# Performance work log

Measured on AMD Instinct MI355X. Metric: run time of the kernel, lower is better.

## Reference

```python
import jax, jax.numpy as jnp
import numpy as np

B, N, K = 8, 2048, 32
EPS = 1e-5


def _lrelu(x):
    return jnp.where(x >= 0, x, 0.2 * x)


def _bn(x, p):
    # inference BatchNorm; x: [B, C, ...], p: [4, C] = (gamma, beta, mean, var)
    g, b, m, v = p[0], p[1], p[2], p[3]
    shape = (1, -1) + (1,) * (x.ndim - 2)
    scale = g * jax.lax.rsqrt(v + EPS)
    return (x - m.reshape(shape)) * scale.reshape(shape) + b.reshape(shape)


def _group(x, k):
    # ops.group with xyz_or_feature='feature', feature_or_diff='diff'
    # x: [B, C, N] -> edge features [B, 2C, N, k] = cat(neighbor - center, center)
    xt = jnp.transpose(x, (0, 2, 1))  # [B, N, C]
    sq = jnp.sum(xt * xt, axis=-1)    # [B, N]
    dist = sq[:, :, None] - 2.0 * jnp.einsum('bnc,bmc->bnm', xt, xt) + sq[:, None, :]
    idx = jax.lax.top_k(-dist, k)[1]  # [B, N, k] nearest neighbors
    nbr = jax.vmap(lambda f, i: f[i])(xt, idx)  # [B, N, k, C]
    center = xt[:, :, None, :]
    edge = jnp.concatenate([nbr - center, jnp.broadcast_to(center, nbr.shape)], axis=-1)
    return jnp.transpose(edge, (0, 3, 1, 2))  # [B, 2C, N, k]


def _edgeconv(x, w1, bn1, w2, bn2, k):
    e = _group(x, k)
    h = _lrelu(_bn(jnp.einsum('oc,bcnk->bonk', w1, e), bn1))
    h = _lrelu(_bn(jnp.einsum('oc,bcnk->bonk', w2, h), bn2))
    return jnp.max(h, axis=-1)  # max over neighbors -> [B, C_out, N]


def _model(x,
           ec1_w1, ec1_bn1, ec1_w2, ec1_bn2,
           ec2_w1, ec2_bn1, ec2_w2, ec2_bn2,
           ec3_w1, ec3_bn1, ec3_w2, ec3_bn2,
           emb_w, q_w, k_w, v_w, att_bn1, ff_w1, ff_w2, att_bn2,
           cb_w, cb_bn):
    # EdgeConvBlock (3 stacked EdgeConvs, outputs concatenated)
    f1 = _edgeconv(x, ec1_w1, ec1_bn1, ec1_w2, ec1_bn2, K)
    f2 = _edgeconv(f1, ec2_w1, ec2_bn1, ec2_w2, ec2_bn2, K)
    f3 = _edgeconv(f2, ec3_w1, ec3_bn1, ec3_w2, ec3_bn2, K)
    xc = jnp.concatenate([f1, f2, f3], axis=1)  # [B, 192, N]
    # Point2PointAttentionBlock: embedding then dense self-attention
    h = jnp.einsum('oc,bcn->bon', emb_w, xc)  # [B, 1024, N]
    q = jnp.einsum('oc,bcn->bon', q_w, h)
    kk = jnp.einsum('oc,bcn->bon', k_w, h)
    v = jnp.einsum('oc,bcn->bon', v_w, h)
    scale = jnp.sqrt(jnp.asarray(h.shape[1], h.dtype))
    att = jax.nn.softmax(jnp.einsum('bcn,bcm->bnm', q, kk) / scale, axis=-1)  # [B, N, N]
    x_r = jnp.einsum('bnm,bcm->bcn', att, v)
    h = _bn(h + x_r, att_bn1)
    ff = jnp.einsum('oc,bcn->bon', ff_w2, _lrelu(jnp.einsum('oc,bcn->bon', ff_w1, h)))
    h = _bn(h + ff, att_bn2)
    # ConvBlock head
    return _lrelu(_bn(jnp.einsum('oc,bcn->bon', cb_w, h), cb_bn))  # [B, 1024, N]


def setup_inputs() -> dict:
    key = jax.random.key(0)
    ks = iter(jax.random.split(key, 32))

    def randn(shape, s=0.1):
        return jax.random.normal(next(ks), shape, jnp.float32) * s

    def bnp(c):
        return jax.random.uniform(next(ks), (4, c), jnp.float32, 0.1, 1.0)

    return {
        'x': randn((B, 3, N), 1.0),
        'ec1_w1': randn((64, 6)), 'ec1_bn1': bnp(64),
        'ec1_w2': randn((64, 64)), 'ec1_bn2': bnp(64),
        'ec2_w1': randn((64, 128)), 'ec2_bn1': bnp(64),
        'ec2_w2': randn((64, 64)), 'ec2_bn2': bnp(64),
        'ec3_w1': randn((64, 128)), 'ec3_bn1': bnp(64),
        'ec3_w2': randn((64, 64)), 'ec3_bn2': bnp(64),
        'emb_w': randn((1024, 192), 0.05),
        'q_w': randn((1024, 1024), 0.03),
        'k_w': randn((1024, 1024), 0.03),
        'v_w': randn((1024, 1024), 0.03),
        'att_bn1': bnp(1024),
        'ff_w1': randn((512, 1024), 0.03),
        'ff_w2': randn((1024, 512), 0.03),
        'att_bn2': bnp(1024),
        'cb_w': randn((1024, 1024), 0.03),
        'cb_bn': bnp(1024),
    }


def reference(x,
              ec1_w1, ec1_bn1, ec1_w2, ec1_bn2,
              ec2_w1, ec2_bn1, ec2_w2, ec2_bn2,
              ec3_w1, ec3_bn1, ec3_w2, ec3_bn2,
              emb_w, q_w, k_w, v_w, att_bn1, ff_w1, ff_w2, att_bn2,
              cb_w, cb_bn):
    return _model(x,
                  ec1_w1, ec1_bn1, ec1_w2, ec1_bn2,
                  ec2_w1, ec2_bn1, ec2_w2, ec2_bn2,
                  ec3_w1, ec3_bn1, ec3_w2, ec3_bn2,
                  emb_w, q_w, k_w, v_w, att_bn1, ff_w1, ff_w2, att_bn2,
                  cb_w, cb_bn)
```

## Files before the change

### kernel.cpp

```cpp
#include <hip/hip_runtime.h>
#include <hip/hip_bf16.h>

constexpr int Bn  = 8;
constexpr int Np  = 2048;
constexpr int KNN = 32;

typedef __attribute__((ext_vector_type(8))) short bf16x8;
typedef __attribute__((ext_vector_type(4))) float f32x4;

__device__ static inline void gll16(const void* g, void* l) {
  __builtin_amdgcn_global_load_lds((const __attribute__((address_space(1))) void*)g,
                                   (__attribute__((address_space(3))) void*)l, 16, 0, 0);
}

__device__ static inline unsigned short f2bf(float x) {
  union { __hip_bfloat16 h; unsigned short u; } cv; cv.h = __float2bfloat16(x); return cv.u;
}
__device__ static inline float bf2f(unsigned short u) {
  union { __hip_bfloat16 h; unsigned short u; } cv; cv.u = u; return __bfloat162float(cv.h);
}

__global__ __launch_bounds__(256)
void cvt_bf16_kernel(const float* __restrict__ s, __hip_bfloat16* __restrict__ d, int n) {
  int i = blockIdx.x * 256 + threadIdx.x;
  if (i < n) d[i] = __float2bfloat16(s[i]);
}

template<int CIN, int K1>
__global__ __launch_bounds__(256)
void cvt_w1a(const float* __restrict__ w1, __hip_bfloat16* __restrict__ out) {
  int i = blockIdx.x * 256 + threadIdx.x;
  if (i >= 64 * K1) return;
  int o = i / K1, c = i - o * K1;
  out[i] = __float2bfloat16(c < CIN ? w1[o * 2 * CIN + c] : 0.f);
}

__global__ __launch_bounds__(256)
void xpose_kernel(const float* __restrict__ x, float* __restrict__ xt,
                  __hip_bfloat16* __restrict__ xb) {
  int i = blockIdx.x * 256 + threadIdx.x;
  int b = i >> 11, n = i & 2047;
  const float* p = x + (long)b * 3 * Np + n;
  float vx = p[0], vy = p[Np], vz = p[2 * Np];
  xt[(long)i * 4 + 0] = vx;
  xt[(long)i * 4 + 1] = vy;
  xt[(long)i * 4 + 2] = vz;
  xt[(long)i * 4 + 3] = 0.f;
  __hip_bfloat16* q = xb + (long)i * 8;
  q[0] = __float2bfloat16(vx); q[1] = __float2bfloat16(vy);
  q[2] = __float2bfloat16(vz);
  q[3] = __float2bfloat16(0.f); q[4] = q[3]; q[5] = q[3]; q[6] = q[3]; q[7] = q[3];
}

template<int C, int CP>
__global__ __launch_bounds__(256)
void sq_kernel(const float* __restrict__ f, float* __restrict__ out) {
  int i = blockIdx.x * 256 + threadIdx.x;
  const float* p = f + (long)i * CP;
  float s = 0.f;
#pragma unroll
  for (int c = 0; c < C; ++c) s += p[c] * p[c];
  out[i] = s;
}

template<int CIN, int CP>
__global__ __launch_bounds__(256)
void split_kernel(const float* __restrict__ f, __hip_bfloat16* __restrict__ fhi,
                  __hip_bfloat16* __restrict__ flo) {
  int i = blockIdx.x * 256 + threadIdx.x;
  int n = i >> 6, c = i & 63;
  float v = (c < CIN) ? f[(long)n * CP + c] : 0.f;
  __hip_bfloat16 h = __float2bfloat16(v);
  fhi[i] = h;
  flo[i] = __float2bfloat16(v - __bfloat162float(h));
}

__device__ static inline unsigned umin32(unsigned a, unsigned b) { return a < b ? a : b; }

__device__ static inline int mbcnt64(unsigned long long m) {
  return __builtin_amdgcn_mbcnt_hi((unsigned)(m >> 32),
         __builtin_amdgcn_mbcnt_lo((unsigned)m, 0u));
}

__device__ static inline unsigned long long shfl64x(unsigned long long k, int m) {
  unsigned lo = (unsigned)__shfl_xor((int)(unsigned)k, m);
  unsigned hi = (unsigned)__shfl_xor((int)(unsigned)(k >> 32), m);
  return ((unsigned long long)hi << 32) | (unsigned long long)lo;
}

__device__ static inline unsigned long long lane_sort64_u64(unsigned long long v, int lane) {
#pragma unroll
  for (int k = 2; k <= 64; k <<= 1) {
#pragma unroll
    for (int j = k >> 1; j > 0; j >>= 1) {
      unsigned long long o = shfl64x(v, j);
      bool dir = ((lane & k) == 0);
      bool lower = ((lane & j) == 0);
      bool keep = (v < o) == (dir == lower);
      v = keep ? v : o;
    }
  }
  return v;
}

__device__ static inline unsigned long long lane_merge64(unsigned long long a,
                                                         unsigned long long b, int lane) {
  unsigned long long br = shfl64x(b, 63);
  unsigned long long m = a < br ? a : br;
#pragma unroll
  for (int j = 32; j > 0; j >>= 1) {
    unsigned long long o = shfl64x(m, j);
    bool lower = ((lane & j) == 0);
    bool keep = (m < o) == lower;
    m = keep ? m : o;
  }
  return m;
}

__device__ static inline unsigned kth_u32(unsigned v, int km1) {
  unsigned p = 0;
#pragma unroll
  for (int b = 31; b >= 0; --b) {
    unsigned t = p | (1u << b);
    if ((int)__popcll(__ballot(v < t)) <= km1) p = t;
  }
  return p;
}

template<int MAP, int CAP>
__device__ static inline void row_topk(const unsigned* val, unsigned long long* cbuf,
                                       int lane, int* outp) {
  unsigned tmn[16];
#pragma unroll
  for (int i = 0; i < 16; ++i) tmn[i] = umin32(val[i], val[i + 16]);
#pragma unroll
  for (int w2 = 8; w2 >= 1; w2 >>= 1)
#pragma unroll
    for (int i = 0; i < 8; ++i)
      if (i < w2) tmn[i] = umin32(tmn[i], tmn[i + w2]);

  unsigned T = kth_u32(tmn[0], 31);

  int S = 0;
#pragma unroll
  for (int s = 0; s < 32; ++s) {
    bool p = val[s] <= T;
    unsigned long long mask = __ballot(p);
    int pos = S + mbcnt64(mask);
    unsigned idx = (MAP == 0) ? (unsigned)((s >> 2) * 256 + lane * 4 + (s & 3))
                              : (unsigned)((s >> 2) * 256 + (s & 3) * 64 + lane);
    if (p && pos < CAP) cbuf[pos] = ((unsigned long long)val[s] << 32) | idx;
    S += (int)__popcll(mask);
  }

  if (S <= 64) {
    unsigned long long k = (lane < S) ? cbuf[lane] : ~0ull;
    unsigned vs = (unsigned)(k >> 32), ix = (unsigned)k;
    unsigned vstar = kth_u32(vs, 31);
    int c1 = (int)__popcll(__ballot(vs < vstar));
    int r = 32 - c1;
    unsigned istar = 0;
#pragma unroll
    for (int b = 10; b >= 0; --b) {
      unsigned t = istar | (1u << b);
      if ((int)__popcll(__ballot(vs == vstar && ix < t)) <= r - 1) istar = t;
    }
    bool sel = (vs < vstar) || (vs == vstar && ix <= istar);
    unsigned long long m = __ballot(sel);
    if (sel) outp[mbcnt64(m)] = (int)ix;
  } else if (S <= CAP) {
    int nslot = (S + 63) >> 6;
    unsigned vs[CAP / 64], is_[CAP / 64];
#pragma unroll
    for (int q = 0; q < CAP / 64; ++q) {
      unsigned long long k = (q * 64 + lane < S) ? cbuf[q * 64 + lane] : ~0ull;
      vs[q] = (unsigned)(k >> 32);
      is_[q] = (unsigned)k;
    }
    unsigned vstar = 0;
#pragma unroll
    for (int b = 31; b >= 0; --b) {
      unsigned t = vstar | (1u << b);
      int c = 0;
      for (int q = 0; q < nslot; ++q) c += (int)__popcll(__ballot(vs[q] < t));
      if (c <= 31) vstar = t;
    }
    int c1 = 0;
    for (int q = 0; q < nslot; ++q) c1 += (int)__popcll(__ballot(vs[q] < vstar));
    int r = 32 - c1;
    unsigned istar = 0;
#pragma unroll
    for (int b = 10; b >= 0; --b) {
      unsigned t = istar | (1u << b);
      int c = 0;
      for (int q = 0; q < nslot; ++q)
        c += (int)__popcll(__ballot(vs[q] == vstar && is_[q] < t));
      if (c <= r - 1) istar = t;
    }
    int base = 0;
    for (int q = 0; q < nslot; ++q) {
      bool sel = (vs[q] < vstar) || (vs[q] == vstar && is_[q] <= istar);
      unsigned long long m = __ballot(sel);
      if (sel) outp[base + mbcnt64(m)] = (int)is_[q];
      base += (int)__popcll(m);
    }
  } else {
    unsigned long long cur = ~0ull;
    for (int s = 0; s < 32; ++s) {
      unsigned idx = (MAP == 0) ? (unsigned)((s >> 2) * 256 + lane * 4 + (s & 3))
                                : (unsigned)((s >> 2) * 256 + (s & 3) * 64 + lane);
      unsigned long long kc = ((unsigned long long)val[s] << 32) | idx;
      cur = lane_merge64(cur, lane_sort64_u64(kc, lane), lane);
    }
    if (lane < KNN) outp[lane] = (int)(unsigned)cur;
  }
}

__global__ __launch_bounds__(512)
void knn3_kernel(const float* __restrict__ xt, const float* __restrict__ sqb,
                 int* __restrict__ idxOut) {
  __shared__ float4 F[2048];
  __shared__ float sqS[2048];
  __shared__ unsigned long long cbuf[8 * 256];
  int t = threadIdx.x, lane = t & 63, w = t >> 6;
  long pb = (long)blockIdx.y * Np;
  for (int e = t; e < 2048; e += 512) {
    F[e] = ((const float4*)xt)[pb + e];
    sqS[e] = sqb[pb + e];
  }
  __syncthreads();
  int row = blockIdx.x * 8 + w;
  float4 a = F[row];
  unsigned val[32];
#pragma unroll
  for (int j4 = 0; j4 < 8; ++j4)
#pragma unroll
    for (int u = 0; u < 4; ++u) {
      int col = j4 * 256 + u * 64 + lane;
      float4 fb = F[col];
      float d = sqS[col] - 2.f * (a.x * fb.x + a.y * fb.y + a.z * fb.z);
      unsigned b = __float_as_uint(d);
      val[j4 * 4 + u] = b ^ ((unsigned)((int)b >> 31) | 0x80000000u);
    }
  row_topk<1, 256>(val, cbuf + w * 256, lane, idxOut + (pb + row) * KNN);
}

__global__ __launch_bounds__(512)
void knn16_kernel(const __hip_bfloat16* __restrict__ fhi,
                  const __hip_bfloat16* __restrict__ flo,
                  const float* __restrict__ sqb, int* __restrict__ idxOut) {
  constexpr int LDW = 2052;
  constexpr int CAP = 256;
  __shared__ __align__(16) float Dw[16 * LDW];
  __shared__ float sqS[2048];
  __shared__ unsigned long long cbuf[8 * CAP];
  int t = threadIdx.x, lane = t & 63, w = t >> 6;
  long pb = (long)blockIdx.y * Np;
  int r0 = blockIdx.x * 16;
  const __hip_bfloat16* fh = fhi + pb * 64;
  const __hip_bfloat16* fl = flo + pb * 64;

  ((float4*)sqS)[t] = ((const float4*)(sqb + pb))[t];

  int ar = r0 + (lane & 15);
  int kc = (lane >> 4) * 8;
  int n15 = lane & 15;
  bf16x8 ah[2], al[2];
#pragma unroll
  for (int k2 = 0; k2 < 2; ++k2) {
    ah[k2] = *(const bf16x8*)(fh + (long)ar * 64 + k2 * 32 + kc);
    al[k2] = *(const bf16x8*)(fl + (long)ar * 64 + k2 * 32 + kc);
  }
  __syncthreads();

  int cb0 = w * 256;
  bf16x8 b0h[2], b0l[2], b1h[2], b1l[2];
  {
    int bc = cb0 + n15;
#pragma unroll
    for (int k2 = 0; k2 < 2; ++k2) {
      b0h[k2] = *(const bf16x8*)(fh + (long)bc * 64 + k2 * 32 + kc);
      b0l[k2] = *(const bf16x8*)(fl + (long)bc * 64 + k2 * 32 + kc);
    }
    bc = cb0 + 16 + n15;
#pragma unroll
    for (int k2 = 0; k2 < 2; ++k2) {
      b1h[k2] = *(const bf16x8*)(fh + (long)bc * 64 + k2 * 32 + kc);
      b1l[k2] = *(const bf16x8*)(fl + (long)bc * 64 + k2 * 32 + kc);
    }
  }
  int m0 = (lane >> 4) * 4;
#pragma unroll
  for (int cp = 0; cp < 8; ++cp) {
    {
      int ct = cp * 2;
      bf16x8 nh[2], nl[2];
      if (ct + 2 < 16) {
        int bc = cb0 + (ct + 2) * 16 + n15;
#pragma unroll
        for (int k2 = 0; k2 < 2; ++k2) {
          nh[k2] = *(const bf16x8*)(fh + (long)bc * 64 + k2 * 32 + kc);
          nl[k2] = *(const bf16x8*)(fl + (long)bc * 64 + k2 * 32 + kc);
        }
      }
      f32x4 acc = f32x4{0.f, 0.f, 0.f, 0.f};
#pragma unroll
      for (int k2 = 0; k2 < 2; ++k2) {
        acc = __builtin_amdgcn_mfma_f32_16x16x32_bf16(ah[k2], b0h[k2], acc, 0, 0, 0);
        acc = __builtin_amdgcn_mfma_f32_16x16x32_bf16(ah[k2], b0l[k2], acc, 0, 0, 0);
        acc = __builtin_amdgcn_mfma_f32_16x16x32_bf16(al[k2], b0h[k2], acc, 0, 0, 0);
      }
      int col = cb0 + ct * 16 + n15;
      float sqv = sqS[col];
#pragma unroll
      for (int r = 0; r < 4; ++r)
        Dw[(m0 + r) * LDW + col] = sqv - 2.f * acc[r];
#pragma unroll
      for (int k2 = 0; k2 < 2; ++k2) { b0h[k2] = nh[k2]; b0l[k2] = nl[k2]; }
    }
    {
      int ct = cp * 2 + 1;
      bf16x8 nh[2], nl[2];
      if (ct + 2 < 16) {
        int bc = cb0 + (ct + 2) * 16 + n15;
#pragma unroll
        for (int k2 = 0; k2 < 2; ++k2) {
          nh[k2] = *(const bf16x8*)(fh + (long)bc * 64 + k2 * 32 + kc);
          nl[k2] = *(const bf16x8*)(fl + (long)bc * 64 + k2 * 32 + kc);
        }
      }
      f32x4 acc = f32x4{0.f, 0.f, 0.f, 0.f};
#pragma unroll
      for (int k2 = 0; k2 < 2; ++k2) {
        acc = __builtin_amdgcn_mfma_f32_16x16x32_bf16(ah[k2], b1h[k2], acc, 0, 0, 0);
        acc = __builtin_amdgcn_mfma_f32_16x16x32_bf16(ah[k2], b1l[k2], acc, 0, 0, 0);
        acc = __builtin_amdgcn_mfma_f32_16x16x32_bf16(al[k2], b1h[k2], acc, 0, 0, 0);
      }
      int col = cb0 + ct * 16 + n15;
      float sqv = sqS[col];
#pragma unroll
      for (int r = 0; r < 4; ++r)
        Dw[(m0 + r) * LDW + col] = sqv - 2.f * acc[r];
#pragma unroll
      for (int k2 = 0; k2 < 2; ++k2) { b1h[k2] = nh[k2]; b1l[k2] = nl[k2]; }
    }
  }
  __syncthreads();

  for (int rr = 0; rr < 2; ++rr) {
    int row = w * 2 + rr;
    unsigned val[32];
    const float4* rp = (const float4*)&Dw[row * LDW];
#pragma unroll
    for (int j4 = 0; j4 < 8; ++j4) {
      float4 f4 = rp[j4 * 64 + lane];
      float fv[4] = {f4.x, f4.y, f4.z, f4.w};
#pragma unroll
      for (int u = 0; u < 4; ++u) {
        unsigned b = __float_as_uint(fv[u]);
        val[j4 * 4 + u] = b ^ ((unsigned)((int)b >> 31) | 0x80000000u);
      }
    }
    row_topk<0, CAP>(val, cbuf + w * CAP, lane, idxOut + (pb + r0 + row) * KNN);
  }
}

template<int CIN, int CP>
__global__ __launch_bounds__(256)
void biasker(const float* __restrict__ feat, const float* __restrict__ w1,
             float* __restrict__ bias) {
  __shared__ float wd[64][CIN + 1];
  int tid = threadIdx.x;
  for (int e = tid; e < 64 * CIN; e += 256) {
    int o = e / CIN, c = e - o * CIN;
    wd[o][c] = w1[o * 2 * CIN + CIN + c] - w1[o * 2 * CIN + c];
  }
  __syncthreads();
  int wv = tid >> 6, o = tid & 63;
  float wr_[CIN];
#pragma unroll
  for (int c = 0; c < CIN; ++c) wr_[c] = wd[o][c];
  long base = (long)blockIdx.y * Np + blockIdx.x * 32 + wv * 8;
  for (int p = 0; p < 8; ++p) {
    const float* fr = feat + (base + p) * CP;
    float acc = 0.f;
#pragma unroll
    for (int c = 0; c < CIN; ++c) acc = fmaf(wr_[c], fr[c], acc);
    bias[(base + p) * 64 + o] = acc;
  }
}

template<int K1>
__global__ __launch_bounds__(256)
void edge_mfma(const __hip_bfloat16* __restrict__ featb, int fstride,
               const int* __restrict__ idx, const float* __restrict__ bias,
               const __hip_bfloat16* __restrict__ w1b,
               const __hip_bfloat16* __restrict__ w2b,
               const float* __restrict__ bn1, const float* __restrict__ bn2,
               float* __restrict__ fout, __hip_bfloat16* __restrict__ xcseg) {
  __shared__ __align__(16) char lds[32768 + 64 * K1 * 2 + 8192 + 1024 + 512];
  __hip_bfloat16* A  = (__hip_bfloat16*)lds;
  __hip_bfloat16* H1 = A + 128 * K1;
  float*          H2 = (float*)lds;
  __hip_bfloat16* W1 = (__hip_bfloat16*)(lds + 32768);
  __hip_bfloat16* W2 = W1 + 64 * K1;
  float* biasS = (float*)(lds + 32768 + 64 * K1 * 2 + 8192);
  int*   idxS  = (int*)(biasS + 256);

  int t = threadIdx.x, lane = t & 63, w = t >> 6;
  long pb = (long)blockIdx.y * Np;
  int p0 = blockIdx.x * 4;

  if (t < 128) idxS[t] = idx[(pb + p0 + (t >> 5)) * KNN + (t & 31)];
  biasS[w * 64 + lane] = bias[(pb + p0 + w) * 64 + lane];
  for (int e = t; e < 64 * K1 / 8; e += 256)
    ((ulonglong2*)W1)[e] = ((const ulonglong2*)w1b)[e];
  for (int e = t; e < 512; e += 256)
    ((ulonglong2*)W2)[e] = ((const ulonglong2*)w2b)[e];
  __syncthreads();

  if (K1 == 64) {
#pragma unroll
    for (int i = 0; i < 4; ++i) {
      int e = t + i * 256;
      int r = e >> 3, cc = e & 7;
      const ulonglong2* src = (const ulonglong2*)(featb + (pb + idxS[r]) * fstride) + cc;
      ((ulonglong2*)(A + r * 64))[cc] = *src;
    }
  } else {
    if (t < 128) {
      int r = t;
      ulonglong2 z; z.x = 0; z.y = 0;
      ((ulonglong2*)(A + r * 32))[0] = *(const ulonglong2*)(featb + (pb + idxS[r]) * fstride);
      ((ulonglong2*)(A + r * 32))[1] = z;
      ((ulonglong2*)(A + r * 32))[2] = z;
      ((ulonglong2*)(A + r * 32))[3] = z;
    }
  }

  int ocol = lane & 15;
  float sc1[4], sh1[4], sc2[4], sh2[4];
#pragma unroll
  for (int jn = 0; jn < 4; ++jn) {
    int o = jn * 16 + ocol;
    sc1[jn] = bn1[o] * rsqrtf(bn1[192 + o] + 1e-5f);
    sh1[jn] = bn1[64 + o] - bn1[128 + o] * sc1[jn];
    sc2[jn] = bn2[o] * rsqrtf(bn2[192 + o] + 1e-5f);
    sh2[jn] = bn2[64 + o] - bn2[128 + o] * sc2[jn];
  }
  __syncthreads();

  int mrow = lane & 15;
  int kc   = (lane >> 4) * 8;
  constexpr int KS = K1 / 32;

  f32x4 acc[2][4];
#pragma unroll
  for (int im = 0; im < 2; ++im)
#pragma unroll
    for (int jn = 0; jn < 4; ++jn) acc[im][jn] = f32x4{0.f, 0.f, 0.f, 0.f};
#pragma unroll
  for (int s = 0; s < KS; ++s) {
    bf16x8 af[2], bf_[4];
#pragma unroll
    for (int im = 0; im < 2; ++im)
      af[im] = *(const bf16x8*)(A + (w * 32 + im * 16 + mrow) * K1 + s * 32 + kc);
#pragma unroll
    for (int jn = 0; jn < 4; ++jn)
      bf_[jn] = *(const bf16x8*)(W1 + (jn * 16 + mrow) * K1 + s * 32 + kc);
#pragma unroll
    for (int im = 0; im < 2; ++im)
#pragma unroll
      for (int jn = 0; jn < 4; ++jn)
        acc[im][jn] = __builtin_amdgcn_mfma_f32_16x16x32_bf16(af[im], bf_[jn], acc[im][jn], 0, 0, 0);
  }
#pragma unroll
  for (int im = 0; im < 2; ++im)
#pragma unroll
    for (int jn = 0; jn < 4; ++jn) {
      int o = jn * 16 + ocol;
      float bsv = biasS[w * 64 + o];
#pragma unroll
      for (int r = 0; r < 4; ++r) {
        int m = w * 32 + im * 16 + (lane >> 4) * 4 + r;
        float x = (acc[im][jn][r] + bsv) * sc1[jn] + sh1[jn];
        x = fmaxf(x, 0.2f * x);
        H1[m * 64 + o] = __float2bfloat16(x);
      }
    }
  __syncthreads();

  bf16x8 a2[2][2], b2[4][2];
#pragma unroll
  for (int im = 0; im < 2; ++im)
#pragma unroll
    for (int s = 0; s < 2; ++s)
      a2[im][s] = *(const bf16x8*)(H1 + (w * 32 + im * 16 + mrow) * 64 + s * 32 + kc);
#pragma unroll
  for (int jn = 0; jn < 4; ++jn)
#pragma unroll
    for (int s = 0; s < 2; ++s)
      b2[jn][s] = *(const bf16x8*)(W2 + (jn * 16 + mrow) * 64 + s * 32 + kc);
  __syncthreads();

  f32x4 acc2[2][4];
#pragma unroll
  for (int im = 0; im < 2; ++im)
#pragma unroll
    for (int jn = 0; jn < 4; ++jn) acc2[im][jn] = f32x4{0.f, 0.f, 0.f, 0.f};
#pragma unroll
  for (int s = 0; s < 2; ++s)
#pragma unroll
    for (int im = 0; im < 2; ++im)
#pragma unroll
      for (int jn = 0; jn < 4; ++jn)
        acc2[im][jn] = __builtin_amdgcn_mfma_f32_16x16x32_bf16(a2[im][s], b2[jn][s], acc2[im][jn], 0, 0, 0);
#pragma unroll
  for (int im = 0; im < 2; ++im)
#pragma unroll
    for (int jn = 0; jn < 4; ++jn) {
      int o = jn * 16 + ocol;
#pragma unroll
      for (int r = 0; r < 4; ++r) {
        int m = w * 32 + im * 16 + (lane >> 4) * 4 + r;
        float x = acc2[im][jn][r] * sc2[jn] + sh2[jn];
        x = fmaxf(x, 0.2f * x);
        H2[m * 64 + o] = x;
      }
    }
  __syncthreads();

  {
    int o = t & 63;
    float m = -3.4e38f;
#pragma unroll
    for (int k = 0; k < 32; ++k) m = fmaxf(m, H2[(w * 32 + k) * 64 + o]);
    int n2 = p0 + w;
    if (fout) fout[(pb + n2) * 64 + o] = m;
    xcseg[(pb + n2) * 192 + o] = __float2bfloat16(m);
  }
}

template<int OUTF, int BNMODE, int RESID, int LRELU>
__global__ __launch_bounds__(512)
void gemm_db(const __hip_bfloat16* __restrict__ A, int lda, long sA,
             const __hip_bfloat16* __restrict__ B, int ldb, long sB,
             void* __restrict__ Cv, int ldc, long sC,
             const __hip_bfloat16* __restrict__ R, long sR,
             const float* __restrict__ bn, int bnlen, int Kd,
             int gx, int gy) {
  int nwg = gx * gy * Bn;
  int cpx = nwg >> 3;
  int orig = blockIdx.x;
  int wg = (orig & 7) * cpx + (orig >> 3);
  int bz = wg / (gx * gy);
  int rem = wg - bz * (gx * gy);
  int by = rem / gx;
  int bx = rem - by * gx;
  A += (long)bz * sA;
  B += (long)bz * sB;
  long i0 = (long)bx * 256, j0 = (long)by * 256;

  __shared__ __hip_bfloat16 As[2][256 * 64];
  __shared__ __hip_bfloat16 Bs[2][256 * 64];

  int t = threadIdx.x, lane = t & 63, w = t >> 6;
  int wm = w & 1, wn = w >> 1;

  f32x4 acc[8][4];
#pragma unroll
  for (int im = 0; im < 8; ++im)
#pragma unroll
    for (int jn = 0; jn < 4; ++jn) acc[im][jn] = f32x4{0.f, 0.f, 0.f, 0.f};

#define STAGE_DB(bi, kt)                                                     \
  {                                                                          \
    _Pragma("unroll")                                                        \
    for (int i = 0; i < 4; ++i) {                                            \
      int e = t + i * 512;                                                   \
      int r = e >> 3, c = e & 7;                                             \
      int cs = c ^ (r & 7);                                                  \
      gll16(A + (i0 + r) * lda + (kt) * 64 + cs * 8,                         \
            (__hip_bfloat16*)As[bi] + e * 8);                                \
    }                                                                        \
    _Pragma("unroll")                                                        \
    for (int i = 0; i < 4; ++i) {                                            \
      int e = t + i * 512;                                                   \
      int r = e >> 3, c = e & 7;                                             \
      int cs = c ^ (r & 7);                                                  \
      gll16(B + (j0 + r) * ldb + (kt) * 64 + cs * 8,                         \
            (__hip_bfloat16*)Bs[bi] + e * 8);                                \
    }                                                                        \
  }

  int nt = Kd >> 6;
  STAGE_DB(0, 0);
  __syncthreads();

  int cur = 0;
  for (int kt = 0; kt < nt; ++kt) {
    if (kt + 1 < nt) STAGE_DB(cur ^ 1, kt + 1);
    const __hip_bfloat16* Ab = As[cur];
    const __hip_bfloat16* Bb = Bs[cur];
#pragma unroll
    for (int ks = 0; ks < 2; ++ks) {
      bf16x8 af[8], bfv[4];
#pragma unroll
      for (int im = 0; im < 8; ++im) {
        int ra = wm * 128 + im * 16 + (lane & 15);
        int q = (ks * 4 + (lane >> 4)) ^ (ra & 7);
        af[im] = *(const bf16x8*)(Ab + ra * 64 + q * 8);
      }
#pragma unroll
      for (int jn = 0; jn < 4; ++jn) {
        int rb = wn * 64 + jn * 16 + (lane & 15);
        int q = (ks * 4 + (lane >> 4)) ^ (rb & 7);
        bfv[jn] = *(const bf16x8*)(Bb + rb * 64 + q * 8);
      }
#pragma unroll
      for (int im = 0; im < 8; ++im)
#pragma unroll
        for (int jn = 0; jn < 4; ++jn)
          acc[im][jn] = __builtin_amdgcn_mfma_f32_16x16x32_bf16(af[im], bfv[jn], acc[im][jn], 0, 0, 0);
    }
    __syncthreads();
    cur ^= 1;
  }
#undef STAGE_DB

  int mlocal = (lane >> 4) * 4;
  int nlocal = lane & 15;
#pragma unroll
  for (int i = 0; i < 8; ++i) {
    long m0 = i0 + wm * 128 + i * 16 + mlocal;
    float bsc[4], bsh[4];
    if (BNMODE == 1) {
#pragma unroll
      for (int r = 0; r < 4; ++r) {
        long c = m0 + r;
        float sc = bn[c] * rsqrtf(bn[3 * bnlen + c] + 1e-5f);
        bsc[r] = sc;
        bsh[r] = bn[bnlen + c] - bn[2 * bnlen + c] * sc;
      }
    }
#pragma unroll
    for (int j = 0; j < 4; ++j) {
      long nn = j0 + wn * 64 + j * 16 + nlocal;
      float sc2 = 1.f, sh2 = 0.f;
      if (BNMODE == 2) {
        sc2 = bn[nn] * rsqrtf(bn[3 * bnlen + nn] + 1e-5f);
        sh2 = bn[bnlen + nn] - bn[2 * bnlen + nn] * sc2;
      }
      f32x4 v = acc[i][j];
      float o4[4];
      ushort4 rv;
      if (RESID) rv = *(const ushort4*)(R + (long)bz * sR + nn * ldc + m0);
#pragma unroll
      for (int r = 0; r < 4; ++r) {
        float x = v[r];
        if (RESID) x += bf2f(r == 0 ? rv.x : r == 1 ? rv.y : r == 2 ? rv.z : rv.w);
        if (BNMODE == 1) x = x * bsc[r] + bsh[r];
        if (BNMODE == 2) x = x * sc2 + sh2;
        if (LRELU) x = (x >= 0.f) ? x : 0.2f * x;
        o4[r] = x;
      }
      if (OUTF) {
        float* Cp = (float*)Cv + (long)bz * sC + nn * ldc + m0;
        *(float4*)Cp = make_float4(o4[0], o4[1], o4[2], o4[3]);
      } else {
        __hip_bfloat16* Cp = (__hip_bfloat16*)Cv + (long)bz * sC + nn * ldc + m0;
        ushort4 sv;
        sv.x = f2bf(o4[0]); sv.y = f2bf(o4[1]); sv.z = f2bf(o4[2]); sv.w = f2bf(o4[3]);
        *(ushort4*)Cp = sv;
      }
    }
  }
}

__global__ __launch_bounds__(256)
void softmax_bf(__hip_bfloat16* __restrict__ S) {
  long row = (long)blockIdx.y * Np + blockIdx.x;
  __hip_bfloat16* p = S + row * Np;
  int t = threadIdx.x;
  const float scale = 0.03125f;
  float v[8];
  float mx = -3.4e38f;
#pragma unroll
  for (int u = 0; u < 8; ++u) {
    v[u] = __bfloat162float(p[u * 256 + t]) * scale;
    mx = fmaxf(mx, v[u]);
  }
  __shared__ float red[4];
#pragma unroll
  for (int off = 32; off > 0; off >>= 1) mx = fmaxf(mx, __shfl_xor(mx, off));
  if ((t & 63) == 0) red[t >> 6] = mx;
  __syncthreads();
  mx = fmaxf(fmaxf(red[0], red[1]), fmaxf(red[2], red[3]));
  __syncthreads();
  float sum = 0.f;
#pragma unroll
  for (int u = 0; u < 8; ++u) { v[u] = __expf(v[u] - mx); sum += v[u]; }
#pragma unroll
  for (int off = 32; off > 0; off >>= 1) sum += __shfl_xor(sum, off);
  if ((t & 63) == 0) red[t >> 6] = sum;
  __syncthreads();
  sum = red[0] + red[1] + red[2] + red[3];
  float inv = 1.f / sum;
#pragma unroll
  for (int u = 0; u < 8; ++u) p[u * 256 + t] = __float2bfloat16(v[u] * inv);
}

extern "C" void kernel_launch(void* const* d_in, const int* in_sizes, int n_in,
                              void* d_out, int out_size, void* d_ws, size_t ws_size,
                              hipStream_t stream) {
  const float* x       = (const float*)d_in[0];
  const float* ec1_w1  = (const float*)d_in[1];
  const float* ec1_bn1 = (const float*)d_in[2];
  const float* ec1_w2  = (const float*)d_in[3];
  const float* ec1_bn2 = (const float*)d_in[4];
  const float* ec2_w1  = (const float*)d_in[5];
  const float* ec2_bn1 = (const float*)d_in[6];
  const float* ec2_w2  = (const float*)d_in[7];
  const float* ec2_bn2 = (const float*)d_in[8];
  const float* ec3_w1  = (const float*)d_in[9];
  const float* ec3_bn1 = (const float*)d_in[10];
  const float* ec3_w2  = (const float*)d_in[11];
  const float* ec3_bn2 = (const float*)d_in[12];
  const float* emb_w   = (const float*)d_in[13];
  const float* q_w     = (const float*)d_in[14];
  const float* k_w     = (const float*)d_in[15];
  const float* v_w     = (const float*)d_in[16];
  const float* att_bn1 = (const float*)d_in[17];
  const float* ff_w1   = (const float*)d_in[18];
  const float* ff_w2   = (const float*)d_in[19];
  const float* att_bn2 = (const float*)d_in[20];
  const float* cb_w    = (const float*)d_in[21];
  const float* cb_bn   = (const float*)d_in[22];
  float* out = (float*)d_out;
  (void)in_sizes; (void)n_in; (void)out_size; (void)ws_size;

  float* ws  = (float*)d_ws;
  float* xt  = ws;
  float* f1  = xt + 65536;
  float* f2  = f1 + 1048576;
  float* sqb = f2 + 1048576;
  int*   idxb = (int*)(sqb + 16384);
  __hip_bfloat16* xc  = (__hip_bfloat16*)(idxb + 524288);
  __hip_bfloat16* wts = xc + 3145728;
  __hip_bfloat16* ew  = wts + 5439488;
  __hip_bfloat16* xb  = ew + 22528;
  float* big = (float*)(xb + 131072);
  __hip_bfloat16* hb  = (__hip_bfloat16*)big;
  __hip_bfloat16* qb  = hb + 16777216;
  __hip_bfloat16* kb  = qb + 16777216;
  __hip_bfloat16* vtb = kb + 16777216;
  __hip_bfloat16* Sb  = vtb + 16777216;
  __hip_bfloat16* fhi = (__hip_bfloat16*)big;
  __hip_bfloat16* flo = fhi + 1048576;
  float* biasb = big + 33554432;

  __hip_bfloat16* emb_wb = wts;
  __hip_bfloat16* q_wb   = wts + 196608;
  __hip_bfloat16* k_wb   = wts + 1245184;
  __hip_bfloat16* v_wb   = wts + 2293760;
  __hip_bfloat16* ff1_wb = wts + 3342336;
  __hip_bfloat16* ff2_wb = wts + 3866624;
  __hip_bfloat16* cb_wb  = wts + 4390912;

  __hip_bfloat16* w1a1_b = ew;
  __hip_bfloat16* w2_1b  = ew + 2048;
  __hip_bfloat16* w1a2_b = ew + 6144;
  __hip_bfloat16* w2_2b  = ew + 10240;
  __hip_bfloat16* w1a3_b = ew + 14336;
  __hip_bfloat16* w2_3b  = ew + 18432;

  const long sN1024 = (long)Np * 1024;
  const long sN512  = (long)Np * 512;
  const long sN192  = (long)Np * 192;
  const long sNN    = (long)Np * Np;

  cvt_bf16_kernel<<<768,  256, 0, stream>>>(emb_w, emb_wb, 196608);
  cvt_bf16_kernel<<<4096, 256, 0, stream>>>(q_w,   q_wb,   1048576);
  cvt_bf16_kernel<<<4096, 256, 0, stream>>>(k_w,   k_wb,   1048576);
  cvt_bf16_kernel<<<4096, 256, 0, stream>>>(v_w,   v_wb,   1048576);
  cvt_bf16_kernel<<<2048, 256, 0, stream>>>(ff_w1, ff1_wb, 524288);
  cvt_bf16_kernel<<<2048, 256, 0, stream>>>(ff_w2, ff2_wb, 524288);
  cvt_bf16_kernel<<<4096, 256, 0, stream>>>(cb_w,  cb_wb,  1048576);
  cvt_w1a<3, 32><<<8, 256, 0, stream>>>(ec1_w1, w1a1_b);
  cvt_w1a<64, 64><<<16, 256, 0, stream>>>(ec2_w1, w1a2_b);
  cvt_w1a<64, 64><<<16, 256, 0, stream>>>(ec3_w1, w1a3_b);
  cvt_bf16_kernel<<<16, 256, 0, stream>>>(ec1_w2, w2_1b, 4096);
  cvt_bf16_kernel<<<16, 256, 0, stream>>>(ec2_w2, w2_2b, 4096);
  cvt_bf16_kernel<<<16, 256, 0, stream>>>(ec3_w2, w2_3b, 4096);

  xpose_kernel<<<64, 256, 0, stream>>>(x, xt, xb);

  sq_kernel<3, 4><<<64, 256, 0, stream>>>(xt, sqb);
  knn3_kernel<<<dim3(Np / 8, Bn), 512, 0, stream>>>(xt, sqb, idxb);
  biasker<3, 4><<<dim3(Np / 32, Bn), 256, 0, stream>>>(xt, ec1_w1, biasb);
  edge_mfma<32><<<dim3(Np / 4, Bn), 256, 0, stream>>>(
      xb, 8, idxb, biasb, w1a1_b, w2_1b, ec1_bn1, ec1_bn2, f1, xc);

  sq_kernel<64, 64><<<64, 256, 0, stream>>>(f1, sqb);
  split_kernel<64, 64><<<4096, 256, 0, stream>>>(f1, fhi, flo);
  knn16_kernel<<<dim3(Np / 16, Bn), 512, 0, stream>>>(fhi, flo, sqb, idxb);
  biasker<64, 64><<<dim3(Np / 32, Bn), 256, 0, stream>>>(f1, ec2_w1, biasb);
  edge_mfma<64><<<dim3(Np / 4, Bn), 256, 0, stream>>>(
      xc, 192, idxb, biasb, w1a2_b, w2_2b, ec2_bn1, ec2_bn2, f2, xc + 64);

  sq_kernel<64, 64><<<64, 256, 0, stream>>>(f2, sqb);
  split_kernel<64, 64><<<4096, 256, 0, stream>>>(f2, fhi, flo);
  knn16_kernel<<<dim3(Np / 16, Bn), 512, 0, stream>>>(fhi, flo, sqb, idxb);
  biasker<64, 64><<<dim3(Np / 32, Bn), 256, 0, stream>>>(f2, ec3_w1, biasb);
  edge_mfma<64><<<dim3(Np / 4, Bn), 256, 0, stream>>>(
      xc + 64, 192, idxb, biasb, w1a3_b, w2_3b, ec3_bn1, ec3_bn2, nullptr, xc + 128);

  gemm_db<0, 0, 0, 0><<<dim3(4 * 8 * Bn), 512, 0, stream>>>(
      emb_wb, 192, 0, xc, 192, sN192, hb, 1024, sN1024, nullptr, 0, nullptr, 0, 192, 4, 8);

  gemm_db<0, 0, 0, 0><<<dim3(4 * 8 * Bn), 512, 0, stream>>>(
      q_wb, 1024, 0, hb, 1024, sN1024, qb, 1024, sN1024, nullptr, 0, nullptr, 0, 1024, 4, 8);
  gemm_db<0, 0, 0, 0><<<dim3(4 * 8 * Bn), 512, 0, stream>>>(
      k_wb, 1024, 0, hb, 1024, sN1024, kb, 1024, sN1024, nullptr, 0, nullptr, 0, 1024, 4, 8);
  gemm_db<0, 0, 0, 0><<<dim3(8 * 4 * Bn), 512, 0, stream>>>(
      hb, 1024, sN1024, v_wb, 1024, 0, vtb, 2048, sN1024, nullptr, 0, nullptr, 0, 1024, 8, 4);

  gemm_db<0, 0, 0, 0><<<dim3(8 * 8 * Bn), 512, 0, stream>>>(
      kb, 1024, sN1024, qb, 1024, sN1024, Sb, 2048, sNN, nullptr, 0, nullptr, 0, 1024, 8, 8);
  softmax_bf<<<dim3(Np, Bn), 256, 0, stream>>>(Sb);

  gemm_db<0, 1, 1, 0><<<dim3(4 * 8 * Bn), 512, 0, stream>>>(
      vtb, 2048, sN1024, Sb, 2048, sNN, hb, 1024, sN1024, hb, sN1024, att_bn1, 1024, 2048, 4, 8);

  gemm_db<0, 0, 0, 1><<<dim3(2 * 8 * Bn), 512, 0, stream>>>(
      ff1_wb, 1024, 0, hb, 1024, sN1024, qb, 512, sN512, nullptr, 0, nullptr, 0, 1024, 2, 8);
  gemm_db<0, 1, 1, 0><<<dim3(4 * 8 * Bn), 512, 0, stream>>>(
      ff2_wb, 512, 0, qb, 512, sN512, hb, 1024, sN1024, hb, sN1024, att_bn2, 1024, 512, 4, 8);

  gemm_db<1, 2, 0, 1><<<dim3(8 * 4 * Bn), 512, 0, stream>>>(
      hb, 1024, sN1024, cb_wb, 1024, 0, out, 2048, sN1024, nullptr, 0, cb_bn, 1024, 1024, 8, 4);
}
```

Baseline: 947.6 us.

## Deepen kNN B-fragment prefetch and interleave GEMM MFMA phases with barriers/setprio

In the kNN distance kernel, the B-operand register prefetch is rewritten as a 4-slot ring with a prefetch distance of four column tiles instead of two. This is meant to hide global-load latency behind the MFMA work. In the main bf16 GEMM, each k-tile is split into four phases that load half of the A fragments, then issue 16 MFMAs between s_barrier calls while wave priority is raised with s_setprio. The goal is to keep waves in lockstep and overlap LDS reads with MFMA work, at the cost of more barriers and, in the kNN kernel, more live registers.

Result: slower. 994.7 us (+5.0%).

```diff
diff --git a/kernel.cpp b/kernel.cpp
--- a/kernel.cpp
+++ b/kernel.cpp
@@ -274,75 +274,39 @@
   __syncthreads();
 
   int cb0 = w * 256;
-  bf16x8 b0h[2], b0l[2], b1h[2], b1l[2];
-  {
-    int bc = cb0 + n15;
+  bf16x8 bh[4][2], bl[4][2];
+#pragma unroll
+  for (int s0 = 0; s0 < 4; ++s0) {
+    int bc = cb0 + s0 * 16 + n15;
 #pragma unroll
     for (int k2 = 0; k2 < 2; ++k2) {
-      b0h[k2] = *(const bf16x8*)(fh + (long)bc * 64 + k2 * 32 + kc);
-      b0l[k2] = *(const bf16x8*)(fl + (long)bc * 64 + k2 * 32 + kc);
-    }
-    bc = cb0 + 16 + n15;
+      bh[s0][k2] = *(const bf16x8*)(fh + (long)bc * 64 + k2 * 32 + kc);
+      bl[s0][k2] = *(const bf16x8*)(fl + (long)bc * 64 + k2 * 32 + kc);
+    }
+  }
+  int m0 = (lane >> 4) * 4;
+#pragma unroll
+  for (int ct = 0; ct < 16; ++ct) {
+    const int sl = ct & 3;
+    f32x4 acc = f32x4{0.f, 0.f, 0.f, 0.f};
 #pragma unroll
     for (int k2 = 0; k2 < 2; ++k2) {
-      b1h[k2] = *(const bf16x8*)(fh + (long)bc * 64 + k2 * 32 + kc);
-      b1l[k2] = *(const bf16x8*)(fl + (long)bc * 64 + k2 * 32 + kc);
-    }
-  }
-  int m0 = (lane >> 4) * 4;
-#pragma unroll
-  for (int cp = 0; cp < 8; ++cp) {
-    {
-      int ct = cp * 2;
-      bf16x8 nh[2], nl[2];
-      if (ct + 2 < 16) {
-        int bc = cb0 + (ct + 2) * 16 + n15;
-#pragma unroll
-        for (int k2 = 0; k2 < 2; ++k2) {
-          nh[k2] = *(const bf16x8*)(fh + (long)bc * 64 + k2 * 32 + kc);
-          nl[k2] = *(const bf16x8*)(fl + (long)bc * 64 + k2 * 32 + kc);
-        }
-      }
-      f32x4 acc = f32x4{0.f, 0.f, 0.f, 0.f};
+      acc = __builtin_amdgcn_mfma_f32_16x16x32_bf16(ah[k2], bh[sl][k2], acc, 0, 0, 0);
+      acc = __builtin_amdgcn_mfma_f32_16x16x32_bf16(ah[k2], bl[sl][k2], acc, 0, 0, 0);
+      acc = __builtin_amdgcn_mfma_f32_16x16x32_bf16(al[k2], bh[sl][k2], acc, 0, 0, 0);
+    }
+    int col = cb0 + ct * 16 + n15;
+    float sqv = sqS[col];
+#pragma unroll
+    for (int r = 0; r < 4; ++r)
+      Dw[(m0 + r) * LDW + col] = sqv - 2.f * acc[r];
+    if (ct + 4 < 16) {
+      int bc = cb0 + (ct + 4) * 16 + n15;
 #pragma unroll
       for (int k2 = 0; k2 < 2; ++k2) {
-        acc = __builtin_amdgcn_mfma_f32_16x16x32_bf16(ah[k2], b0h[k2], acc, 0, 0, 0);
-        acc = __builtin_amdgcn_mfma_f32_16x16x32_bf16(ah[k2], b0l[k2], acc, 0, 0, 0);
-        acc = __builtin_amdgcn_mfma_f32_16x16x32_bf16(al[k2], b0h[k2], acc, 0, 0, 0);
-      }
-      int col = cb0 + ct * 16 + n15;
-      float sqv = sqS[col];
-#pragma unroll
-      for (int r = 0; r < 4; ++r)
-        Dw[(m0 + r) * LDW + col] = sqv - 2.f * acc[r];
-#pragma unroll
-      for (int k2 = 0; k2 < 2; ++k2) { b0h[k2] = nh[k2]; b0l[k2] = nl[k2]; }
-    }
-    {
-      int ct = cp * 2 + 1;
-      bf16x8 nh[2], nl[2];
-      if (ct + 2 < 16) {
-        int bc = cb0 + (ct + 2) * 16 + n15;
-#pragma unroll
-        for (int k2 = 0; k2 < 2; ++k2) {
-          nh[k2] = *(const bf16x8*)(fh + (long)bc * 64 + k2 * 32 + kc);
-          nl[k2] = *(const bf16x8*)(fl + (long)bc * 64 + k2 * 32 + kc);
-        }
-      }
-      f32x4 acc = f32x4{0.f, 0.f, 0.f, 0.f};
-#pragma unroll
-      for (int k2 = 0; k2 < 2; ++k2) {
-        acc = __builtin_amdgcn_mfma_f32_16x16x32_bf16(ah[k2], b1h[k2], acc, 0, 0, 0);
-        acc = __builtin_amdgcn_mfma_f32_16x16x32_bf16(ah[k2], b1l[k2], acc, 0, 0, 0);
-        acc = __builtin_amdgcn_mfma_f32_16x16x32_bf16(al[k2], b1h[k2], acc, 0, 0, 0);
-      }
-      int col = cb0 + ct * 16 + n15;
-      float sqv = sqS[col];
-#pragma unroll
-      for (int r = 0; r < 4; ++r)
-        Dw[(m0 + r) * LDW + col] = sqv - 2.f * acc[r];
-#pragma unroll
-      for (int k2 = 0; k2 < 2; ++k2) { b1h[k2] = nh[k2]; b1l[k2] = nl[k2]; }
+        bh[sl][k2] = *(const bf16x8*)(fh + (long)bc * 64 + k2 * 32 + kc);
+        bl[sl][k2] = *(const bf16x8*)(fl + (long)bc * 64 + k2 * 32 + kc);
+      }
     }
   }
   __syncthreads();
@@ -602,26 +566,36 @@
     if (kt + 1 < nt) STAGE_DB(cur ^ 1, kt + 1);
     const __hip_bfloat16* Ab = As[cur];
     const __hip_bfloat16* Bb = Bs[cur];
-#pragma unroll
-    for (int ks = 0; ks < 2; ++ks) {
-      bf16x8 af[8], bfv[4];
-#pragma unroll
-      for (int im = 0; im < 8; ++im) {
+    bf16x8 bk[4];
+#pragma unroll
+    for (int p = 0; p < 4; ++p) {
+      const int ks = p >> 1, imh = p & 1;
+      if (imh == 0) {
+#pragma unroll
+        for (int jn = 0; jn < 4; ++jn) {
+          int rb = wn * 64 + jn * 16 + (lane & 15);
+          int q = (ks * 4 + (lane >> 4)) ^ (rb & 7);
+          bk[jn] = *(const bf16x8*)(Bb + rb * 64 + q * 8);
+        }
+      }
+      bf16x8 af4[4];
+#pragma unroll
+      for (int i4 = 0; i4 < 4; ++i4) {
+        int im = imh * 4 + i4;
         int ra = wm * 128 + im * 16 + (lane & 15);
         int q = (ks * 4 + (lane >> 4)) ^ (ra & 7);
-        af[im] = *(const bf16x8*)(Ab + ra * 64 + q * 8);
-      }
-#pragma unroll
-      for (int jn = 0; jn < 4; ++jn) {
-        int rb = wn * 64 + jn * 16 + (lane & 15);
-        int q = (ks * 4 + (lane >> 4)) ^ (rb & 7);
-        bfv[jn] = *(const bf16x8*)(Bb + rb * 64 + q * 8);
-      }
-#pragma unroll
-      for (int im = 0; im < 8; ++im)
+        af4[i4] = *(const bf16x8*)(Ab + ra * 64 + q * 8);
+      }
+      __builtin_amdgcn_s_barrier();
+      __builtin_amdgcn_s_setprio(1);
+#pragma unroll
+      for (int i4 = 0; i4 < 4; ++i4)
 #pragma unroll
         for (int jn = 0; jn < 4; ++jn)
-          acc[im][jn] = __builtin_amdgcn_mfma_f32_16x16x32_bf16(af[im], bfv[jn], acc[im][jn], 0, 0, 0);
+          acc[imh * 4 + i4][jn] = __builtin_amdgcn_mfma_f32_16x16x32_bf16(
+              af4[i4], bk[jn], acc[imh * 4 + i4][jn], 0, 0, 0);
+      __builtin_amdgcn_s_setprio(0);
+      __builtin_amdgcn_s_barrier();
     }
     __syncthreads();
     cur ^= 1;
```
